# Kernel optimization log

Hardware: AMD Instinct MI355X
Metric: run time of the kernel (lower is better)

## Reference

```python
import jax, jax.numpy as jnp
import numpy as np

VOXEL_SIZE = (0.2, 0.2)
GX, GY = 512, 512
MAX_PTS = 32  # max_points_per_pillar
IN_CH = 4


def setup_inputs() -> dict:
    key = jax.random.key(0)
    k1, k2 = jax.random.split(key)
    N, B = 400000, 2
    extent = GX * VOXEL_SIZE[0]  # 102.4 -> points land inside the grid
    all_points = jax.random.uniform(k1, (N, IN_CH), dtype=jnp.float32) * extent
    batch_indices = jnp.sort(jax.random.randint(k2, (N,), 0, B))
    return {"all_points": all_points, "batch_indices": batch_indices, "num_point_clouds": B}


def reference(all_points, batch_indices, num_point_clouds):
    B, P, C = num_point_clouds, MAX_PTS, all_points.shape[1]
    G = B * GX * GY  # total pillar slots
    vs = jnp.array(VOXEL_SIZE, dtype=all_points.dtype)
    # torch .long() truncates toward zero; points are non-negative here
    xy = (all_points[:, :2] / vs).astype(jnp.int32)
    xy = jnp.clip(xy, 0, jnp.array([GX - 1, GY - 1], dtype=jnp.int32))
    bidx = batch_indices.astype(jnp.int32)
    flat = bidx * (GX * GY) + xy[:, 0] * GY + xy[:, 1]  # [N]
    # counts per pillar (torch.unique + scatter_add equivalent)
    counts_full = jax.ops.segment_sum(jnp.ones_like(flat), flat, num_segments=G)
    occupied = counts_full > 0
    # torch.unique inverse index = rank of the pillar among occupied pillars
    inverse_full = jnp.cumsum(occupied.astype(jnp.int32)) - 1  # [G]
    inverse = inverse_full[flat]                               # [N]
    # drop ALL points of over-full pillars (count > P), as the original mask does
    mask = counts_full[flat] <= P
    pos = jnp.arange(flat.shape[0], dtype=jnp.int32)
    last_pos = jax.ops.segment_max(jnp.where(mask, pos, -1), inverse, num_segments=G)
    occ = last_pos >= 0
    winner = jnp.where(occ[:, None], all_points[jnp.clip(last_pos, 0)], 0.0)  # [G, C]
    # [M,C] assigned into [M,P,C] broadcasts over the P slot dim in torch
    voxel_features = jnp.broadcast_to(winner[:, None, :], (G, P, C)).reshape(B, GX, GY, P, C)
    # original allocates voxel_counts but never writes it
    voxel_counts = jnp.zeros((B, GX, GY), dtype=jnp.int32)
    return voxel_features, voxel_counts
```

## Files before the change

kernel.cpp:

```cpp
#include <hip/hip_runtime.h>

#define GXv 512
#define GYv 512
#define PMAX 32

typedef float vfloat4 __attribute__((ext_vector_type(4)));
typedef int   vint4   __attribute__((ext_vector_type(4)));

__global__ void zero_kernel(vint4* __restrict__ counts4, int n4) {
    int i = blockIdx.x * blockDim.x + threadIdx.x;
    if (i < n4) counts4[i] = (vint4)0;
}

__global__ void points_kernel(const float4* __restrict__ pts, const int* __restrict__ bidx,
                              int* __restrict__ counts, int* __restrict__ lastp, int N) {
    int i = blockIdx.x * blockDim.x + threadIdx.x;
    if (i >= N) return;
    float4 p = pts[i];
    int x = (int)(p.x / 0.2f);
    int y = (int)(p.y / 0.2f);
    x = min(max(x, 0), GXv - 1);
    y = min(max(y, 0), GYv - 1);
    int flat = bidx[i] * (GXv * GYv) + x * GYv + y;
    atomicAdd(&counts[flat], 1);
    atomicMax(&lastp[flat], i + 1);
}

__global__ void blocksum_kernel(const int* __restrict__ counts, int* __restrict__ bs) {
    int t = threadIdx.x, b = blockIdx.x;
    int2 c = ((const int2*)counts)[b * 256 + t];
    __shared__ int sm[256];
    sm[t] = (c.x > 0) + (c.y > 0);
    __syncthreads();
    for (int off = 128; off > 0; off >>= 1) {
        if (t < off) sm[t] += sm[t + off];
        __syncthreads();
    }
    if (t == 0) bs[b] = sm[0];
}

__global__ void scan_kernel(int* __restrict__ bs, int nb) {
    __shared__ int sm[1024];
    int t = threadIdx.x;
    int v = (t < nb) ? bs[t] : 0;
    sm[t] = v;
    __syncthreads();
    for (int off = 1; off < 1024; off <<= 1) {
        int a = (t >= off) ? sm[t - off] : 0;
        __syncthreads();
        sm[t] += a;
        __syncthreads();
    }
    if (t < nb) bs[t] = (t == 0) ? 0 : sm[t - 1];
    if (t == nb - 1) bs[nb] = sm[t];
}

__global__ __launch_bounds__(256) void scatter_kernel(
        const int* __restrict__ counts, const int* __restrict__ lastp,
        const int* __restrict__ bs, const vfloat4* __restrict__ pts,
        vfloat4* __restrict__ out, int G, int SB) {
    __shared__ int sm[256];
    __shared__ vfloat4 pil[512];
    int t = threadIdx.x, b = blockIdx.x;
    int2 c2 = ((const int2*)counts)[b * 256 + t];
    int2 lp2 = ((const int2*)lastp)[b * 256 + t];
    int occ0 = (c2.x > 0), occ1 = (c2.y > 0);

    sm[t] = occ0 + occ1;
    __syncthreads();
    for (int off = 1; off < 256; off <<= 1) {
        int a = (t >= off) ? sm[t - off] : 0;
        __syncthreads();
        sm[t] += a;
        __syncthreads();
    }
    int excl = (t == 0) ? 0 : sm[t - 1];
    int agg = sm[255];

    if (occ0) pil[excl]        = (c2.x <= PMAX) ? pts[lp2.x - 1] : (vfloat4)0;
    if (occ1) pil[excl + occ0] = (c2.y <= PMAX) ? pts[lp2.y - 1] : (vfloat4)0;
    __syncthreads();

    size_t base = (size_t)bs[b] * 32;
    int n = agg * 32;
    for (int j = t; j < n; j += 256) {
        vfloat4 v = pil[j >> 5];
        __builtin_nontemporal_store(v, &out[base + (size_t)j]);
    }

    int M = bs[SB];
    size_t idx = (size_t)M * 32 + (size_t)b * 256 + t;
    size_t end = (size_t)G * 32 + (size_t)(G / 4);
    size_t stride = (size_t)SB * 256;
    vfloat4 z = (vfloat4)0;
    for (; idx < end; idx += stride)
        __builtin_nontemporal_store(z, &out[idx]);
}

extern "C" void kernel_launch(void* const* d_in, const int* in_sizes, int n_in,
                              void* d_out, int out_size, void* d_ws, size_t ws_size,
                              hipStream_t stream) {
    const float4* pts = (const float4*)d_in[0];
    const int* bidx = (const int*)d_in[1];
    int N = in_sizes[0] / 4;
    int G = out_size / 129;
    int SB = G / 512;

    int* counts = (int*)d_ws;
    int* lastp = counts + G;
    int* bs = lastp + G;
    vfloat4* out = (vfloat4*)d_out;

    int n4 = G / 4;
    zero_kernel<<<(n4 + 255) / 256, 256, 0, stream>>>((vint4*)counts, n4);
    points_kernel<<<(N + 255) / 256, 256, 0, stream>>>(pts, bidx, counts, lastp, N);
    blocksum_kernel<<<SB, 256, 0, stream>>>(counts, bs);
    scan_kernel<<<1, 1024, 0, stream>>>(bs, SB);
    scatter_kernel<<<SB, 256, 0, stream>>>(counts, lastp, bs, (const vfloat4*)pts, out, G, SB);
}
```

Measured before the change: 320.5 us.

## Fuse block-sum and scan into scatter via grid barrier; interleave count/lastp

Drops the separate blocksum and scan kernels. Each scatter block publishes its occupied-pillar count, then spins on a global atomic barrier and computes its own prefix offset and the total by reducing the published counts. Counts and last-point indices are also interleaved so that one int4 load serves two pillars. This removes two launches and their gaps, but it depends on all SB=1024 blocks being co-resident to avoid deadlock, and every block redundantly sums the per-block counts.

```diff
diff --git a/kernel.cpp b/kernel.cpp
--- a/kernel.cpp
+++ b/kernel.cpp
@@ -7,13 +7,15 @@
 typedef float vfloat4 __attribute__((ext_vector_type(4)));
 typedef int   vint4   __attribute__((ext_vector_type(4)));
 
-__global__ void zero_kernel(vint4* __restrict__ counts4, int n4) {
+
+__global__ void zero_kernel(vint4* __restrict__ cl4, int n4, int* __restrict__ bar) {
     int i = blockIdx.x * blockDim.x + threadIdx.x;
-    if (i < n4) counts4[i] = (vint4)0;
+    if (i < n4) cl4[i] = (vint4)0;
+    if (i == 0) *bar = 0;
 }
 
 __global__ void points_kernel(const float4* __restrict__ pts, const int* __restrict__ bidx,
-                              int* __restrict__ counts, int* __restrict__ lastp, int N) {
+                              int* __restrict__ cl, int N) {
     int i = blockIdx.x * blockDim.x + threadIdx.x;
     if (i >= N) return;
     float4 p = pts[i];
@@ -22,49 +24,21 @@
     x = min(max(x, 0), GXv - 1);
     y = min(max(y, 0), GYv - 1);
     int flat = bidx[i] * (GXv * GYv) + x * GYv + y;
-    atomicAdd(&counts[flat], 1);
-    atomicMax(&lastp[flat], i + 1);
-}
-
-__global__ void blocksum_kernel(const int* __restrict__ counts, int* __restrict__ bs) {
-    int t = threadIdx.x, b = blockIdx.x;
-    int2 c = ((const int2*)counts)[b * 256 + t];
-    __shared__ int sm[256];
-    sm[t] = (c.x > 0) + (c.y > 0);
-    __syncthreads();
-    for (int off = 128; off > 0; off >>= 1) {
-        if (t < off) sm[t] += sm[t + off];
-        __syncthreads();
-    }
-    if (t == 0) bs[b] = sm[0];
-}
-
-__global__ void scan_kernel(int* __restrict__ bs, int nb) {
-    __shared__ int sm[1024];
-    int t = threadIdx.x;
-    int v = (t < nb) ? bs[t] : 0;
-    sm[t] = v;
-    __syncthreads();
-    for (int off = 1; off < 1024; off <<= 1) {
-        int a = (t >= off) ? sm[t - off] : 0;
-        __syncthreads();
-        sm[t] += a;
-        __syncthreads();
-    }
-    if (t < nb) bs[t] = (t == 0) ? 0 : sm[t - 1];
-    if (t == nb - 1) bs[nb] = sm[t];
+    atomicAdd(&cl[2 * flat], 1);
+    atomicMax(&cl[2 * flat + 1], i + 1);
 }
 
 __global__ __launch_bounds__(256) void scatter_kernel(
-        const int* __restrict__ counts, const int* __restrict__ lastp,
-        const int* __restrict__ bs, const vfloat4* __restrict__ pts,
-        vfloat4* __restrict__ out, int G, int SB) {
+        const int* __restrict__ cl, int* __restrict__ bar, int* __restrict__ agg,
+        const vfloat4* __restrict__ pts, vfloat4* __restrict__ out, int G, int SB) {
     __shared__ int sm[256];
+    __shared__ int smb[256];
     __shared__ vfloat4 pil[512];
     int t = threadIdx.x, b = blockIdx.x;
-    int2 c2 = ((const int2*)counts)[b * 256 + t];
-    int2 lp2 = ((const int2*)lastp)[b * 256 + t];
-    int occ0 = (c2.x > 0), occ1 = (c2.y > 0);
+
+    int4 q = ((const int4*)cl)[b * 256 + t];
+    int cnt0 = q.x, lp0 = q.y, cnt1 = q.z, lp1 = q.w;
+    int occ0 = (cnt0 > 0), occ1 = (cnt1 > 0);
 
     sm[t] = occ0 + occ1;
     __syncthreads();
@@ -75,20 +49,45 @@
         __syncthreads();
     }
     int excl = (t == 0) ? 0 : sm[t - 1];
-    int agg = sm[255];
+    int aggL = sm[255];
 
-    if (occ0) pil[excl]        = (c2.x <= PMAX) ? pts[lp2.x - 1] : (vfloat4)0;
-    if (occ1) pil[excl + occ0] = (c2.y <= PMAX) ? pts[lp2.y - 1] : (vfloat4)0;
+    if (t == 0) {
+        agg[b] = aggL;
+        __threadfence();
+        __hip_atomic_fetch_add(bar, 1, __ATOMIC_RELEASE, __HIP_MEMORY_SCOPE_AGENT);
+    }
+
+    if (occ0) pil[excl]        = (cnt0 <= PMAX) ? pts[lp0 - 1] : (vfloat4)0;
+    if (occ1) pil[excl + occ0] = (cnt1 <= PMAX) ? pts[lp1 - 1] : (vfloat4)0;
+
+    if (t == 0) {
+        while (__hip_atomic_load(bar, __ATOMIC_ACQUIRE, __HIP_MEMORY_SCOPE_AGENT) < SB)
+            __builtin_amdgcn_s_sleep(2);
+    }
     __syncthreads();
 
-    size_t base = (size_t)bs[b] * 32;
-    int n = agg * 32;
+    int s_all = 0, s_below = 0;
+    for (int i = t; i < SB; i += 256) {
+        int v = agg[i];
+        s_all += v;
+        if (i < b) s_below += v;
+    }
+    sm[t] = s_all;
+    smb[t] = s_below;
+    __syncthreads();
+    for (int off = 128; off > 0; off >>= 1) {
+        if (t < off) { sm[t] += sm[t + off]; smb[t] += smb[t + off]; }
+        __syncthreads();
+    }
+    int M = sm[0];
+    size_t base = (size_t)smb[0] * 32;
+
+    int n = aggL * 32;
     for (int j = t; j < n; j += 256) {
         vfloat4 v = pil[j >> 5];
         __builtin_nontemporal_store(v, &out[base + (size_t)j]);
     }
 
-    int M = bs[SB];
     size_t idx = (size_t)M * 32 + (size_t)b * 256 + t;
     size_t end = (size_t)G * 32 + (size_t)(G / 4);
     size_t stride = (size_t)SB * 256;
@@ -106,15 +105,13 @@
     int G = out_size / 129;
     int SB = G / 512;
 
-    int* counts = (int*)d_ws;
-    int* lastp = counts + G;
-    int* bs = lastp + G;
+    int* cl = (int*)d_ws;
+    int* bar = cl + 2 * G;
+    int* agg = bar + 1;
     vfloat4* out = (vfloat4*)d_out;
 
-    int n4 = G / 4;
-    zero_kernel<<<(n4 + 255) / 256, 256, 0, stream>>>((vint4*)counts, n4);
-    points_kernel<<<(N + 255) / 256, 256, 0, stream>>>(pts, bidx, counts, lastp, N);
-    blocksum_kernel<<<SB, 256, 0, stream>>>(counts, bs);
-    scan_kernel<<<1, 1024, 0, stream>>>(bs, SB);
-    scatter_kernel<<<SB, 256, 0, stream>>>(counts, lastp, bs, (const vfloat4*)pts, out, G, SB);
+    int n4 = (2 * G) / 4;
+    zero_kernel<<<(n4 + 255) / 256, 256, 0, stream>>>((vint4*)cl, n4, bar);
+    points_kernel<<<(N + 255) / 256, 256, 0, stream>>>(pts, bidx, cl, N);
+    scatter_kernel<<<SB, 256, 0, stream>>>(cl, bar, agg, (const vfloat4*)pts, out, G, SB);
 }
```

Measured after the change: 391.0 us. +22.0%, slower.
